# Kernel optimization log

Measured on AMD Instinct MI355X. Metric: run time of the kernel, lower is better.

## Reference

```python
import jax, jax.numpy as jnp
import numpy as np

B = 8
N = 2048  # max_seqlen
H = 4
D = 64  # attention_dim
V = 64  # linear_dim
SEQ_LEN = 1024  # tokens per sequence
L = B * SEQ_LEN


def setup_inputs() -> dict:
    key = jax.random.key(0)
    kq, kk, kv, kc = jax.random.split(key, 4)
    tq = jax.random.normal(kq, (L, H * D), dtype=jnp.float32)
    tk = jax.random.normal(kk, (L, H * D), dtype=jnp.float32)
    tv = jax.random.normal(kv, (L, H * V), dtype=jnp.float32)
    offsets = (jnp.arange(B + 1, dtype=jnp.int64) * SEQ_LEN)
    num_candidates = jax.random.randint(kc, (B,), 1, 64, dtype=jnp.int32)
    return {
        "tq": tq, "tk": tk, "tv": tv,
        "offsets": offsets,
        "num_candidates": num_candidates,
        "max_seqlen": N,
        "num_contextuals": 8,
    }


def _valid_attn_mask(n, seq_lengths, num_targets, num_contextuals_vec, target_group_size=1):
    # Port of _get_valid_attn_mask (causal=True, max_attn_len=None, tensor contextuals).
    ids = jnp.arange(n)[None, :]                         # (1, N)
    max_ids = seq_lengths[:, None, None]                 # (B, 1, 1)
    ids = jnp.maximum(ids - num_contextuals_vec[:, None] + 1, 0)   # (B, N)
    max_ids = max_ids - num_contextuals_vec[:, None, None] + 1
    row = ids[:, :, None]                                # (B, N, N) row_ids
    col = ids[:, None, :]                                # col_ids
    dist = row - col
    valid = jnp.eye(n, dtype=bool)[None] | (dist > 0)    # causal
    # target-group mask
    tg = jnp.maximum(ids - max_ids[:, :, 0] + num_targets[:, None], -1) // target_group_size  # (B, N)
    tg_row = tg[:, :, None]
    tg_col = tg[:, None, :]
    tgm = (tg_row == tg_col) | (tg_row < 0) | (tg_col < 0)
    valid = valid & tgm
    max_ids = max_ids - num_targets[:, None, None]
    # contextual rows attend to everything before (adjusted) max_ids
    valid = valid | ((row == 0) & (col < max_ids))
    return valid


def reference(tq, tk, tv, offsets, num_candidates, max_seqlen, num_contextuals):
    n = max_seqlen
    alpha = 1.0 / (D ** 0.5)
    scaling = float(max_seqlen)  # scaling_seqlen == -1 -> max_seqlen
    l = tq.shape[0]
    b = offsets.shape[0] - 1

    q = tq.reshape(l, H, D)
    k = tk.reshape(l, H, D)
    v = tv.reshape(l, H, V)

    tok = jnp.arange(l)
    batch_idx = jnp.searchsorted(offsets, tok, side="right") - 1   # (L,)
    pos = tok - offsets[batch_idx]                                  # (L,)

    def pad(x):  # jagged -> (B, N, H, d)
        return jnp.zeros((b, n, H, x.shape[-1]), x.dtype).at[batch_idx, pos].set(x)

    pq, pk, pv = pad(q), pad(k), pad(v)

    scores = jnp.einsum("bxhd,byhd->bhxy", pq, pk) * alpha
    attn = jax.nn.silu(scores) / scaling

    seq_lengths = offsets[1:] - offsets[:-1]
    nc_vec = jnp.full((b,), num_contextuals, dtype=jnp.int32)
    mask = _valid_attn_mask(n, seq_lengths, num_candidates, nc_vec)
    attn = attn * mask[:, None].astype(attn.dtype)

    out = jnp.einsum("bhxy,byhv->bxhv", attn, pv)   # (B, N, H, V)
    jagged = out[batch_idx, pos]                     # (L, H, V)
    return jagged.reshape(l, H * V)
```

## Files before the change

### kernel.cpp

```cpp
#include <hip/hip_runtime.h>
#include <hip/hip_bf16.h>

typedef __attribute__((ext_vector_type(8))) short s16x8;
typedef __attribute__((ext_vector_type(4))) float f32x4;
typedef __attribute__((ext_vector_type(4))) unsigned short u16x4;
typedef __attribute__((ext_vector_type(4))) float fl4;

__device__ __forceinline__ unsigned short f2bf(float f) {
  union { __hip_bfloat16 b; unsigned short u; } cv;
  cv.b = __float2bfloat16(f);
  return cv.u;
}

__global__ __launch_bounds__(256)
void hstu_fwd(const float* __restrict__ tq, const float* __restrict__ tk,
              const float* __restrict__ tv, const int* __restrict__ ncand,
              float* __restrict__ out)
{
  const int bid = (int)blockIdx.x;
  const int bh  = bid & 31;
  const int jp  = bid >> 5;
  const int qtile = (jp & 1) ? (15 - (jp >> 1)) : (jp >> 1);
  const int b = bh >> 2, h = bh & 3;
  const int tid = (int)threadIdx.x;
  const int w  = tid >> 6;
  const int l  = tid & 63;
  const int rl = l & 15;
  const int g  = l >> 4;
  const int T  = 1024 - ncand[b];
  const int qbase = qtile << 6;

  __shared__ unsigned short Qlds[4096];
  __shared__ unsigned short Klds[4096];
  __shared__ unsigned short Vp[4096];

  const int sy  = tid >> 2;
  const int sq4 = tid & 3;
  const int ssw = (sy & 7) << 4;
  const int vg  = tid >> 6;
  const int vc  = tid & 63;

  {
    const float* src = tq + ((size_t)(b*1024 + qbase + sy))*256 + h*64;
    char* row = (char*)Qlds + sy*128;
#pragma unroll
    for (int j2 = 0; j2 < 4; ++j2) {
      fl4 v = *(const fl4*)(src + (sq4 + 4*j2)*4);
      u16x4 p;
      p[0] = f2bf(v[0]*0.125f); p[1] = f2bf(v[1]*0.125f);
      p[2] = f2bf(v[2]*0.125f); p[3] = f2bf(v[3]*0.125f);
      *(u16x4*)(row + (((sq4 + 4*j2)*8) ^ ssw)) = p;
    }
  }
  __syncthreads();

  s16x8 qf0, qf1;
  {
    const int qr = w*16 + rl;
    const char* base = (const char*)Qlds + qr*128;
    const int sw = (qr & 7) << 4;
    qf0 = *(const s16x8*)(base + ((g*16) ^ sw));
    qf1 = *(const s16x8*)(base + ((64 + g*16) ^ sw));
  }

  f32x4 zero = {0.f, 0.f, 0.f, 0.f};
  f32x4 oacc[4];
#pragma unroll
  for (int i = 0; i < 4; ++i) oacc[i] = zero;

  const int rq = qbase + w*16 + rl;
  const int nkv = (qtile == 0) ? 16 : (qtile + 1);

  for (int kv = 0; kv < nkv; ++kv) {
    {
      const float* src = tk + ((size_t)(b*1024 + kv*64 + sy))*256 + h*64;
      char* row = (char*)Klds + sy*128;
#pragma unroll
      for (int j2 = 0; j2 < 4; ++j2) {
        fl4 v = *(const fl4*)(src + (sq4 + 4*j2)*4);
        u16x4 p;
        p[0] = f2bf(v[0]); p[1] = f2bf(v[1]);
        p[2] = f2bf(v[2]); p[3] = f2bf(v[3]);
        *(u16x4*)(row + (((sq4 + 4*j2)*8) ^ ssw)) = p;
      }
    }
    {
      const float* src = tv + ((size_t)(b*1024 + kv*64))*256 + h*64 + vc;
#pragma unroll
      for (int kp = 0; kp < 2; ++kp)
#pragma unroll
        for (int tu = 0; tu < 2; ++tu) {
          const int y0 = 32*kp + 16*tu + 4*vg;
          u16x4 p;
#pragma unroll
          for (int j2 = 0; j2 < 4; ++j2)
            p[j2] = f2bf(src[(size_t)(y0 + j2)*256] * 4.8828125e-4f);
          *(u16x4*)&Vp[(((kp*4 + vg)*64 + vc)*8 + 4*tu)] = p;
        }
    }
    __syncthreads();

    if (qtile != 0 || kv == 0 || w == 0) {
      f32x4 sacc[4];
#pragma unroll
      for (int i = 0; i < 4; ++i) sacc[i] = zero;
#pragma unroll
      for (int t4 = 0; t4 < 4; ++t4) {
        const int kr = t4*16 + rl;
        const char* base = (const char*)Klds + kr*128;
        const int sw = (kr & 7) << 4;
        s16x8 kf0 = *(const s16x8*)(base + ((g*16) ^ sw));
        s16x8 kf1 = *(const s16x8*)(base + ((64 + g*16) ^ sw));
        sacc[t4] = __builtin_amdgcn_mfma_f32_16x16x32_bf16(kf0, qf0, sacc[t4], 0, 0, 0);
        sacc[t4] = __builtin_amdgcn_mfma_f32_16x16x32_bf16(kf1, qf1, sacc[t4], 0, 0, 0);
      }
      s16x8 pa0, pa1;
#pragma unroll
      for (int t4 = 0; t4 < 4; ++t4) {
#pragma unroll
        for (int r = 0; r < 4; ++r) {
          const int y = kv*64 + t4*16 + 4*g + r;
          const float s = sacc[t4][r];
          const float sig = __builtin_amdgcn_rcpf(1.f + __expf(-s));
          const bool valid = (rq < 8) ? (y < T)
                           : ((y <= rq) && ((rq < T) || (y < T) || (y == rq)));
          const float a = valid ? s * sig : 0.f;
          const short bv = (short)f2bf(a);
          if (t4 < 2) pa0[(t4 & 1)*4 + r] = bv;
          else        pa1[(t4 & 1)*4 + r] = bv;
        }
      }
#pragma unroll
      for (int vt = 0; vt < 4; ++vt) {
        const s16x8 vf0 = *(const s16x8*)&Vp[((0*4 + g)*64 + vt*16 + rl)*8];
        oacc[vt] = __builtin_amdgcn_mfma_f32_16x16x32_bf16(pa0, vf0, oacc[vt], 0, 0, 0);
        const s16x8 vf1 = *(const s16x8*)&Vp[((1*4 + g)*64 + vt*16 + rl)*8];
        oacc[vt] = __builtin_amdgcn_mfma_f32_16x16x32_bf16(pa1, vf1, oacc[vt], 0, 0, 0);
      }
    }
    __syncthreads();
  }

  float* dst = out + ((size_t)(b*1024 + qbase + w*16))*256 + h*64;
#pragma unroll
  for (int vt = 0; vt < 4; ++vt)
#pragma unroll
    for (int r = 0; r < 4; ++r)
      dst[(size_t)(4*g + r)*256 + vt*16 + rl] = oacc[vt][r];
}

extern "C" void kernel_launch(void* const* d_in, const int* in_sizes, int n_in,
                              void* d_out, int out_size, void* d_ws, size_t ws_size,
                              hipStream_t stream) {
  (void)in_sizes; (void)n_in; (void)out_size; (void)d_ws; (void)ws_size;
  const float* tq = (const float*)d_in[0];
  const float* tk = (const float*)d_in[1];
  const float* tv = (const float*)d_in[2];
  const int*   nc = (const int*)d_in[4];
  float* out = (float*)d_out;
  hipLaunchKernelGGL(hstu_fwd, dim3(512), dim3(256), 0, stream, tq, tk, tv, nc, out);
}
```

Measured before the change: 37.69 us.

## Precast Q/K/V to bf16 tiles in a prep kernel and double-buffer async LDS loads

Adds a prep kernel that converts Q, K and V once to bf16 in the swizzled and packed tile layouts and writes them to workspace. The main kernel then streams K/V tiles into double-buffered LDS with direct global-to-LDS loads, prefetching the next tile while computing the current one. It also changes the q-tile block ordering. This removes the repeated fp32 loads and conversions of K/V in every q-tile block, at the cost of a second launch and an extra workspace round trip.

After: 43.00 us. 1.14x slower.

```diff
diff --git a/kernel.cpp b/kernel.cpp
--- a/kernel.cpp
+++ b/kernel.cpp
@@ -12,46 +12,95 @@
   return cv.u;
 }
 
+__device__ __forceinline__ void gl_lds16(const void* g, void* l) {
+  __builtin_amdgcn_global_load_lds(
+      (const __attribute__((address_space(1))) unsigned int*)g,
+      (__attribute__((address_space(3))) unsigned int*)l, 16, 0, 0);
+}
+
 __global__ __launch_bounds__(256)
-void hstu_fwd(const float* __restrict__ tq, const float* __restrict__ tk,
-              const float* __restrict__ tv, const int* __restrict__ ncand,
-              float* __restrict__ out)
+void prep_all(const float* __restrict__ tq, const float* __restrict__ tk,
+              const float* __restrict__ tv, unsigned short* __restrict__ ws)
 {
-  const int bid = (int)blockIdx.x;
-  const int bh  = bid & 31;
-  const int jp  = bid >> 5;
-  const int qtile = (jp & 1) ? (15 - (jp >> 1)) : (jp >> 1);
+  const int bid  = (int)blockIdx.x;
+  const int role = bid >> 9;
+  const int blk  = bid & 511;
+  const int bh = blk >> 4, t = blk & 15;
   const int b = bh >> 2, h = bh & 3;
   const int tid = (int)threadIdx.x;
-  const int w  = tid >> 6;
-  const int l  = tid & 63;
-  const int rl = l & 15;
-  const int g  = l >> 4;
-  const int T  = 1024 - ncand[b];
-  const int qbase = qtile << 6;
+  unsigned short* dst = ws + (size_t)role * 2097152 + (size_t)blk * 4096;
 
-  __shared__ unsigned short Qlds[4096];
-  __shared__ unsigned short Klds[4096];
-  __shared__ unsigned short Vp[4096];
-
-  const int sy  = tid >> 2;
-  const int sq4 = tid & 3;
-  const int ssw = (sy & 7) << 4;
-  const int vg  = tid >> 6;
-  const int vc  = tid & 63;
-
-  {
-    const float* src = tq + ((size_t)(b*1024 + qbase + sy))*256 + h*64;
-    char* row = (char*)Qlds + sy*128;
+  if (role < 2) {
+    const int sy = tid >> 2, sq4 = tid & 3;
+    const float* src = (role ? tq : tk) + ((size_t)(b*1024 + t*64 + sy))*256 + h*64;
+    const float scale = role ? 0.125f : 1.0f;
+    char* row = (char*)dst + sy*128;
+    const int ssw = (sy & 7) << 4;
 #pragma unroll
     for (int j2 = 0; j2 < 4; ++j2) {
       fl4 v = *(const fl4*)(src + (sq4 + 4*j2)*4);
       u16x4 p;
-      p[0] = f2bf(v[0]*0.125f); p[1] = f2bf(v[1]*0.125f);
-      p[2] = f2bf(v[2]*0.125f); p[3] = f2bf(v[3]*0.125f);
+      p[0] = f2bf(v[0]*scale); p[1] = f2bf(v[1]*scale);
+      p[2] = f2bf(v[2]*scale); p[3] = f2bf(v[3]*scale);
       *(u16x4*)(row + (((sq4 + 4*j2)*8) ^ ssw)) = p;
     }
+  } else {
+    const int vg = tid >> 6, vc = tid & 63;
+    const float* src = tv + ((size_t)(b*1024 + t*64))*256 + h*64 + vc;
+#pragma unroll
+    for (int kp = 0; kp < 2; ++kp)
+#pragma unroll
+      for (int tu = 0; tu < 2; ++tu) {
+        const int y0 = 32*kp + 16*tu + 4*vg;
+        u16x4 p;
+#pragma unroll
+        for (int j2 = 0; j2 < 4; ++j2)
+          p[j2] = f2bf(src[(size_t)(y0 + j2)*256] * 4.8828125e-4f);
+        *(u16x4*)&dst[((kp*4 + vg)*64 + vc)*8 + 4*tu] = p;
+      }
   }
+}
+
+__global__ __launch_bounds__(256)
+void hstu_main(const unsigned short* __restrict__ Kb, const unsigned short* __restrict__ Qb,
+               const unsigned short* __restrict__ Vb, const int* __restrict__ ncand,
+               float* __restrict__ out)
+{
+  const int bid = (int)blockIdx.x;
+  const int bh = bid & 31;
+  const int jp = bid >> 5;
+  const int qtile = (jp == 0) ? 0 : (jp == 8) ? 1 : (jp < 8 ? jp + 1 : 24 - jp);
+  const int b = bh >> 2, h = bh & 3;
+  const int tid = (int)threadIdx.x;
+  const int w = tid >> 6, l = tid & 63;
+  const int rl = l & 15, g = l >> 4;
+  const int T = 1024 - ncand[b];
+  const int qbase = qtile << 6;
+
+  __shared__ unsigned short Qlds[4096];
+  __shared__ unsigned short Klds[2][4096];
+  __shared__ unsigned short Vlds[2][4096];
+
+  const char* kt  = (const char*)(Kb + (size_t)bh * 16 * 4096);
+  const char* vtb = (const char*)(Vb + (size_t)bh * 16 * 4096);
+
+  {
+    const char* qs = (const char*)(Qb + ((size_t)bh*16 + qtile)*4096) + w*2048 + l*16;
+    char* qd = (char*)Qlds + w*2048;
+    gl_lds16(qs, qd);
+    gl_lds16(qs + 1024, qd + 1024);
+  }
+
+  auto stage = [&](int buf, int kv) {
+    const char* ks = kt + (size_t)kv*8192 + w*2048 + l*16;
+    char* kd = (char*)Klds[buf] + w*2048;
+    gl_lds16(ks, kd); gl_lds16(ks + 1024, kd + 1024);
+    const char* vs = vtb + (size_t)kv*8192 + w*2048 + l*16;
+    char* vd = (char*)Vlds[buf] + w*2048;
+    gl_lds16(vs, vd); gl_lds16(vs + 1024, vd + 1024);
+  };
+
+  stage(0, 0);
   __syncthreads();
 
   s16x8 qf0, qf1;
@@ -71,43 +120,19 @@
   const int rq = qbase + w*16 + rl;
   const int nkv = (qtile == 0) ? 16 : (qtile + 1);
 
-  for (int kv = 0; kv < nkv; ++kv) {
-    {
-      const float* src = tk + ((size_t)(b*1024 + kv*64 + sy))*256 + h*64;
-      char* row = (char*)Klds + sy*128;
-#pragma unroll
-      for (int j2 = 0; j2 < 4; ++j2) {
-        fl4 v = *(const fl4*)(src + (sq4 + 4*j2)*4);
-        u16x4 p;
-        p[0] = f2bf(v[0]); p[1] = f2bf(v[1]);
-        p[2] = f2bf(v[2]); p[3] = f2bf(v[3]);
-        *(u16x4*)(row + (((sq4 + 4*j2)*8) ^ ssw)) = p;
-      }
-    }
-    {
-      const float* src = tv + ((size_t)(b*1024 + kv*64))*256 + h*64 + vc;
-#pragma unroll
-      for (int kp = 0; kp < 2; ++kp)
-#pragma unroll
-        for (int tu = 0; tu < 2; ++tu) {
-          const int y0 = 32*kp + 16*tu + 4*vg;
-          u16x4 p;
-#pragma unroll
-          for (int j2 = 0; j2 < 4; ++j2)
-            p[j2] = f2bf(src[(size_t)(y0 + j2)*256] * 4.8828125e-4f);
-          *(u16x4*)&Vp[(((kp*4 + vg)*64 + vc)*8 + 4*tu)] = p;
-        }
-    }
-    __syncthreads();
+  for (int t = 0; t < nkv; ++t) {
+    const int cur = t & 1;
+    if (t + 1 < nkv) stage(cur ^ 1, t + 1);
 
-    if (qtile != 0 || kv == 0 || w == 0) {
+    if (qtile != 0 || t == 0 || w == 0) {
       f32x4 sacc[4];
 #pragma unroll
       for (int i = 0; i < 4; ++i) sacc[i] = zero;
+      const char* kb = (const char*)Klds[cur];
 #pragma unroll
       for (int t4 = 0; t4 < 4; ++t4) {
         const int kr = t4*16 + rl;
-        const char* base = (const char*)Klds + kr*128;
+        const char* base = kb + kr*128;
         const int sw = (kr & 7) << 4;
         s16x8 kf0 = *(const s16x8*)(base + ((g*16) ^ sw));
         s16x8 kf1 = *(const s16x8*)(base + ((64 + g*16) ^ sw));
@@ -119,7 +144,7 @@
       for (int t4 = 0; t4 < 4; ++t4) {
 #pragma unroll
         for (int r = 0; r < 4; ++r) {
-          const int y = kv*64 + t4*16 + 4*g + r;
+          const int y = t*64 + t4*16 + 4*g + r;
           const float s = sacc[t4][r];
           const float sig = __builtin_amdgcn_rcpf(1.f + __expf(-s));
           const bool valid = (rq < 8) ? (y < T)
@@ -130,11 +155,12 @@
           else        pa1[(t4 & 1)*4 + r] = bv;
         }
       }
+      const unsigned short* vb = Vlds[cur];
 #pragma unroll
       for (int vt = 0; vt < 4; ++vt) {
-        const s16x8 vf0 = *(const s16x8*)&Vp[((0*4 + g)*64 + vt*16 + rl)*8];
+        const s16x8 vf0 = *(const s16x8*)&vb[((0*4 + g)*64 + vt*16 + rl)*8];
         oacc[vt] = __builtin_amdgcn_mfma_f32_16x16x32_bf16(pa0, vf0, oacc[vt], 0, 0, 0);
-        const s16x8 vf1 = *(const s16x8*)&Vp[((1*4 + g)*64 + vt*16 + rl)*8];
+        const s16x8 vf1 = *(const s16x8*)&vb[((1*4 + g)*64 + vt*16 + rl)*8];
         oacc[vt] = __builtin_amdgcn_mfma_f32_16x16x32_bf16(pa1, vf1, oacc[vt], 0, 0, 0);
       }
     }
@@ -152,11 +178,17 @@
 extern "C" void kernel_launch(void* const* d_in, const int* in_sizes, int n_in,
                               void* d_out, int out_size, void* d_ws, size_t ws_size,
                               hipStream_t stream) {
-  (void)in_sizes; (void)n_in; (void)out_size; (void)d_ws; (void)ws_size;
+  (void)in_sizes; (void)n_in; (void)out_size; (void)ws_size;
   const float* tq = (const float*)d_in[0];
   const float* tk = (const float*)d_in[1];
   const float* tv = (const float*)d_in[2];
   const int*   nc = (const int*)d_in[4];
   float* out = (float*)d_out;
-  hipLaunchKernelGGL(hstu_fwd, dim3(512), dim3(256), 0, stream, tq, tk, tv, nc, out);
+  unsigned short* ws = (unsigned short*)d_ws;
+
+  hipLaunchKernelGGL(prep_all, dim3(1536), dim3(256), 0, stream, tq, tk, tv, ws);
+  const unsigned short* Kb = ws;
+  const unsigned short* Qb = ws + 2097152;
+  const unsigned short* Vb = ws + 4194304;
+  hipLaunchKernelGGL(hstu_main, dim3(512), dim3(256), 0, stream, Kb, Qb, Vb, nc, out);
 }
```

## Split KV range across two wave-pairs with 32-row query tiles and LDS reduction

Applied to the files above, without the earlier changes.

Query tiles shrink from 64 to 32 rows and the grid doubles to 1024 blocks. Within a block, two pairs of waves each process half of the KV tiles into separate LDS buffers, and the partial outputs are summed through shared memory at the end. Q fragments are loaded straight from global memory into registers rather than staged through LDS. The change also adds s_setprio around the MFMA sections and a min-blocks launch bound. It aims to improve parallelism and load balance, at the cost of more redundant K/V loading across blocks and an extra reduction step.

Result: slower. 53.94 us (+43.1%).

```diff
diff --git a/kernel.cpp b/kernel.cpp
--- a/kernel.cpp
+++ b/kernel.cpp
@@ -2,6 +2,7 @@
 #include <hip/hip_bf16.h>
 
 typedef __attribute__((ext_vector_type(8))) short s16x8;
+typedef __attribute__((ext_vector_type(8))) unsigned short u16x8;
 typedef __attribute__((ext_vector_type(4))) float f32x4;
 typedef __attribute__((ext_vector_type(4))) unsigned short u16x4;
 typedef __attribute__((ext_vector_type(4))) float fl4;
@@ -12,55 +13,47 @@
   return cv.u;
 }
 
-__global__ __launch_bounds__(256)
-void hstu_fwd(const float* __restrict__ tq, const float* __restrict__ tk,
-              const float* __restrict__ tv, const int* __restrict__ ncand,
-              float* __restrict__ out)
+__global__ __launch_bounds__(256, 4)
+void hstu_fused(const float* __restrict__ tq, const float* __restrict__ tk,
+                const float* __restrict__ tv, const int* __restrict__ ncand,
+                float* __restrict__ out)
 {
   const int bid = (int)blockIdx.x;
   const int bh  = bid & 31;
-  const int jp  = bid >> 5;
-  const int qtile = (jp & 1) ? (15 - (jp >> 1)) : (jp >> 1);
+  const int qg  = 31 - (bid >> 5);
   const int b = bh >> 2, h = bh & 3;
   const int tid = (int)threadIdx.x;
-  const int w  = tid >> 6;
-  const int l  = tid & 63;
-  const int rl = l & 15;
-  const int g  = l >> 4;
-  const int T  = 1024 - ncand[b];
-  const int qbase = qtile << 6;
+  const int w   = tid >> 6;
+  const int sub = w & 1;
+  const int hf  = w >> 1;
+  const int l   = tid & 63;
+  const int rl  = l & 15, g = l >> 4;
+  const int T   = 1024 - ncand[b];
+  const int qr  = qg*32 + sub*16;
+  const int rq  = qr + rl;
 
-  __shared__ unsigned short Qlds[4096];
-  __shared__ unsigned short Klds[4096];
-  __shared__ unsigned short Vp[4096];
+  __shared__ unsigned short S[16384];
+  unsigned short* KH = S + hf*8192;
+  unsigned short* VH = KH + 4096;
 
-  const int sy  = tid >> 2;
-  const int sq4 = tid & 3;
-  const int ssw = (sy & 7) << 4;
-  const int vg  = tid >> 6;
-  const int vc  = tid & 63;
-
-  {
-    const float* src = tq + ((size_t)(b*1024 + qbase + sy))*256 + h*64;
-    char* row = (char*)Qlds + sy*128;
-#pragma unroll
-    for (int j2 = 0; j2 < 4; ++j2) {
-      fl4 v = *(const fl4*)(src + (sq4 + 4*j2)*4);
-      u16x4 p;
-      p[0] = f2bf(v[0]*0.125f); p[1] = f2bf(v[1]*0.125f);
-      p[2] = f2bf(v[2]*0.125f); p[3] = f2bf(v[3]*0.125f);
-      *(u16x4*)(row + (((sq4 + 4*j2)*8) ^ ssw)) = p;
-    }
-  }
-  __syncthreads();
+  const int pt = sub*64 + l;
+  const int sy = pt >> 1, sq = pt & 1;
+  const int vc = pt & 63, vq = pt >> 6;
 
   s16x8 qf0, qf1;
   {
-    const int qr = w*16 + rl;
-    const char* base = (const char*)Qlds + qr*128;
-    const int sw = (qr & 7) << 4;
-    qf0 = *(const s16x8*)(base + ((g*16) ^ sw));
-    qf1 = *(const s16x8*)(base + ((64 + g*16) ^ sw));
+    const float* qs = tq + ((size_t)(b*1024 + rq))*256 + h*64;
+    fl4 a  = *(const fl4*)(qs + g*8);
+    fl4 b2 = *(const fl4*)(qs + g*8 + 4);
+    fl4 c  = *(const fl4*)(qs + 32 + g*8);
+    fl4 d2 = *(const fl4*)(qs + 36 + g*8);
+#pragma unroll
+    for (int j = 0; j < 4; ++j) {
+      qf0[j]   = (short)f2bf(a[j]  * 0.125f);
+      qf0[j+4] = (short)f2bf(b2[j] * 0.125f);
+      qf1[j]   = (short)f2bf(c[j]  * 0.125f);
+      qf1[j+4] = (short)f2bf(d2[j] * 0.125f);
+    }
   }
 
   f32x4 zero = {0.f, 0.f, 0.f, 0.f};
@@ -68,58 +61,65 @@
 #pragma unroll
   for (int i = 0; i < 4; ++i) oacc[i] = zero;
 
-  const int rq = qbase + w*16 + rl;
-  const int nkv = (qtile == 0) ? 16 : (qtile + 1);
+  const int nkv = (qg == 0) ? 16 : (qg >> 1) + 1;
+  const int nh  = (nkv + 1) >> 1;
 
-  for (int kv = 0; kv < nkv; ++kv) {
-    {
-      const float* src = tk + ((size_t)(b*1024 + kv*64 + sy))*256 + h*64;
-      char* row = (char*)Klds + sy*128;
+  for (int it = 0; it < nh; ++it) {
+    const int t = hf*nh + it;
+    const bool act = (t < nkv);
+    if (act) {
+      const float* ks = tk + ((size_t)(b*1024 + t*64 + sy))*256 + h*64 + sq*32;
+      char* krow = (char*)KH + sy*128;
+      const int ssw = (sy & 7) << 4;
 #pragma unroll
       for (int j2 = 0; j2 < 4; ++j2) {
-        fl4 v = *(const fl4*)(src + (sq4 + 4*j2)*4);
-        u16x4 p;
-        p[0] = f2bf(v[0]); p[1] = f2bf(v[1]);
-        p[2] = f2bf(v[2]); p[3] = f2bf(v[3]);
-        *(u16x4*)(row + (((sq4 + 4*j2)*8) ^ ssw)) = p;
+        fl4 v0 = *(const fl4*)(ks + j2*8);
+        fl4 v1 = *(const fl4*)(ks + j2*8 + 4);
+        u16x8 p;
+#pragma unroll
+        for (int j = 0; j < 4; ++j) { p[j] = f2bf(v0[j]); p[j+4] = f2bf(v1[j]); }
+        *(u16x8*)(krow + (((sq*4 + j2)*16) ^ ssw)) = p;
       }
-    }
-    {
-      const float* src = tv + ((size_t)(b*1024 + kv*64))*256 + h*64 + vc;
+      const float* vs = tv + ((size_t)(b*1024 + t*64))*256 + h*64 + vc;
 #pragma unroll
       for (int kp = 0; kp < 2; ++kp)
 #pragma unroll
-        for (int tu = 0; tu < 2; ++tu) {
-          const int y0 = 32*kp + 16*tu + 4*vg;
-          u16x4 p;
+        for (int tu = 0; tu < 2; ++tu)
 #pragma unroll
-          for (int j2 = 0; j2 < 4; ++j2)
-            p[j2] = f2bf(src[(size_t)(y0 + j2)*256] * 4.8828125e-4f);
-          *(u16x4*)&Vp[(((kp*4 + vg)*64 + vc)*8 + 4*tu)] = p;
-        }
+          for (int gq = 0; gq < 2; ++gq) {
+            const int gg = vq*2 + gq;
+            const int y0 = kp*32 + tu*16 + gg*4;
+            u16x4 p;
+#pragma unroll
+            for (int j = 0; j < 4; ++j)
+              p[j] = f2bf(vs[(size_t)(y0 + j)*256] * 4.8828125e-4f);
+            *(u16x4*)&VH[((kp*4 + gg)*64 + vc)*8 + tu*4] = p;
+          }
     }
     __syncthreads();
 
-    if (qtile != 0 || kv == 0 || w == 0) {
+    if (act) {
       f32x4 sacc[4];
 #pragma unroll
       for (int i = 0; i < 4; ++i) sacc[i] = zero;
+      __builtin_amdgcn_s_setprio(1);
 #pragma unroll
       for (int t4 = 0; t4 < 4; ++t4) {
         const int kr = t4*16 + rl;
-        const char* base = (const char*)Klds + kr*128;
+        const char* base = (const char*)KH + kr*128;
         const int sw = (kr & 7) << 4;
         s16x8 kf0 = *(const s16x8*)(base + ((g*16) ^ sw));
         s16x8 kf1 = *(const s16x8*)(base + ((64 + g*16) ^ sw));
         sacc[t4] = __builtin_amdgcn_mfma_f32_16x16x32_bf16(kf0, qf0, sacc[t4], 0, 0, 0);
         sacc[t4] = __builtin_amdgcn_mfma_f32_16x16x32_bf16(kf1, qf1, sacc[t4], 0, 0, 0);
       }
+      __builtin_amdgcn_s_setprio(0);
       s16x8 pa0, pa1;
 #pragma unroll
       for (int t4 = 0; t4 < 4; ++t4) {
 #pragma unroll
         for (int r = 0; r < 4; ++r) {
-          const int y = kv*64 + t4*16 + 4*g + r;
+          const int y = t*64 + t4*16 + 4*g + r;
           const float s = sacc[t4][r];
           const float sig = __builtin_amdgcn_rcpf(1.f + __expf(-s));
           const bool valid = (rq < 8) ? (y < T)
@@ -130,23 +130,37 @@
           else        pa1[(t4 & 1)*4 + r] = bv;
         }
       }
+      __builtin_amdgcn_s_setprio(1);
 #pragma unroll
       for (int vt = 0; vt < 4; ++vt) {
-        const s16x8 vf0 = *(const s16x8*)&Vp[((0*4 + g)*64 + vt*16 + rl)*8];
+        const s16x8 vf0 = *(const s16x8*)&VH[((0*4 + g)*64 + vt*16 + rl)*8];
         oacc[vt] = __builtin_amdgcn_mfma_f32_16x16x32_bf16(pa0, vf0, oacc[vt], 0, 0, 0);
-        const s16x8 vf1 = *(const s16x8*)&Vp[((1*4 + g)*64 + vt*16 + rl)*8];
+        const s16x8 vf1 = *(const s16x8*)&VH[((1*4 + g)*64 + vt*16 + rl)*8];
         oacc[vt] = __builtin_amdgcn_mfma_f32_16x16x32_bf16(pa1, vf1, oacc[vt], 0, 0, 0);
       }
+      __builtin_amdgcn_s_setprio(0);
     }
     __syncthreads();
   }
 
-  float* dst = out + ((size_t)(b*1024 + qbase + w*16))*256 + h*64;
+  float* Ored = (float*)S;
+  if (hf == 1) {
 #pragma unroll
-  for (int vt = 0; vt < 4; ++vt)
+    for (int vt = 0; vt < 4; ++vt)
 #pragma unroll
-    for (int r = 0; r < 4; ++r)
-      dst[(size_t)(4*g + r)*256 + vt*16 + rl] = oacc[vt][r];
+      for (int r = 0; r < 4; ++r)
+        Ored[sub*1024 + (4*g + r)*64 + vt*16 + rl] = oacc[vt][r];
+  }
+  __syncthreads();
+  if (hf == 0) {
+    float* dst = out + ((size_t)(b*1024 + qr))*256 + h*64;
+#pragma unroll
+    for (int vt = 0; vt < 4; ++vt)
+#pragma unroll
+      for (int r = 0; r < 4; ++r)
+        dst[(size_t)(4*g + r)*256 + vt*16 + rl] =
+            oacc[vt][r] + Ored[sub*1024 + (4*g + r)*64 + vt*16 + rl];
+  }
 }
 
 extern "C" void kernel_launch(void* const* d_in, const int* in_sizes, int n_in,
@@ -158,5 +172,5 @@
   const float* tv = (const float*)d_in[2];
   const int*   nc = (const int*)d_in[4];
   float* out = (float*)d_out;
-  hipLaunchKernelGGL(hstu_fwd, dim3(512), dim3(256), 0, stream, tq, tk, tv, nc, out);
+  hipLaunchKernelGGL(hstu_fused, dim3(1024), dim3(256), 0, stream, tq, tk, tv, nc, out);
 }
```
